# Optimization experiments

Hardware: AMD Instinct MI355X
Metric: run time of the kernel (lower is better)

Reference implementation:

```python
import jax, jax.numpy as jnp
import numpy as np

NUM_HEADS = 16

def setup_inputs() -> dict:
    key = jax.random.key(0)
    ks = jax.random.split(key, 11)
    S, B, E = 2048, 2, 1024
    scale = 1.0 / np.sqrt(E)
    return {
        "query": jax.random.normal(ks[0], (S, B, E), dtype=jnp.float32),
        "key":   jax.random.normal(ks[1], (S, B, E), dtype=jnp.float32),
        "value": jax.random.normal(ks[2], (S, B, E), dtype=jnp.float32),
        "Wq": jax.random.normal(ks[3], (E, E), dtype=jnp.float32) * scale,
        "bq": jax.random.normal(ks[4], (E,), dtype=jnp.float32) * 0.02,
        "Wk": jax.random.normal(ks[5], (E, E), dtype=jnp.float32) * scale,
        "bk": jax.random.normal(ks[6], (E,), dtype=jnp.float32) * 0.02,
        "Wv": jax.random.normal(ks[7], (E, E), dtype=jnp.float32) * scale,
        "bv": jax.random.normal(ks[8], (E,), dtype=jnp.float32) * 0.02,
        "Wo": jax.random.normal(ks[9], (E, E), dtype=jnp.float32) * scale,
        "bo": jax.random.normal(ks[10], (E,), dtype=jnp.float32) * 0.02,
    }

def _batch_invariant_softmax(x):
    # max-shift, exp in input dtype, sum/divide in float32, cast back
    x_max = jnp.max(x, axis=-1, keepdims=True)
    exp_x = jnp.exp(x - x_max).astype(jnp.float32)
    return (exp_x / jnp.sum(exp_x, axis=-1, keepdims=True)).astype(x.dtype)

def reference(query, key, value, Wq, bq, Wk, bk, Wv, bv, Wo, bo):
    S, B, E = query.shape
    H = NUM_HEADS
    D = E // H
    scale = 1.0 / np.sqrt(D)
    # projections (torch Linear: y = x @ W.T + b)
    q = query @ Wq.T + bq   # [S,B,E]
    k = key   @ Wk.T + bk
    v = value @ Wv.T + bv
    # [S,B,E] -> [B,H,S,D]
    q = q.reshape(S, B, H, D).transpose(1, 2, 0, 3)
    k = k.reshape(-1, B, H, D).transpose(1, 2, 0, 3)
    v = v.reshape(-1, B, H, D).transpose(1, 2, 0, 3)
    scores = jnp.einsum('bhqd,bhkd->bhqk', q, k) * scale  # [B,H,S,S]
    causal = jnp.triu(jnp.ones((S, S), dtype=bool), k=1)
    scores = jnp.where(causal, -jnp.inf, scores)
    attn = _batch_invariant_softmax(scores)
    out = jnp.einsum('bhqk,bhkd->bhqd', attn, v)  # [B,H,S,D]
    out = out.transpose(2, 0, 1, 3).reshape(S, B, E)  # [S,B,E]
    return out @ Wo.T + bo
```

## Files before the change

kernel.cpp:

```cpp
#include <hip/hip_runtime.h>
#include <cstddef>
#include <cstdint>

#define S_LEN 2048
#define B_SZ  2
#define E_SZ  1024
#define H_NUM 16
#define D_HEAD 64
#define M_ROWS 4096
#define NEG_BIG (-1e30f)

typedef __attribute__((ext_vector_type(8))) short bf16x8;
typedef __attribute__((ext_vector_type(4))) float f32x4;

#define P_QRYH (0ull << 20)
#define P_QRYL (8ull << 20)
#define P_KEYH (16ull << 20)
#define P_KEYL (24ull << 20)
#define P_VALH (32ull << 20)
#define P_VALL (40ull << 20)
#define P_WQH  (48ull << 20)
#define P_WQL  (50ull << 20)
#define P_WKH  (52ull << 20)
#define P_WKL  (54ull << 20)
#define P_WVH  (56ull << 20)
#define P_WVL  (58ull << 20)
#define P_WOH  (60ull << 20)
#define P_WOL  (62ull << 20)
#define P_QPH  (64ull << 20)
#define P_QPL  (72ull << 20)
#define P_KPH  (80ull << 20)
#define P_KPL  (88ull << 20)
#define P_VTH  (96ull << 20)
#define P_VTL  (104ull << 20)
#define P_AOH  (0ull << 20)
#define P_AOL  (8ull << 20)

__device__ __forceinline__ unsigned short rtne_bf16(float f) {
    unsigned int u = __float_as_uint(f);
    return (unsigned short)((u + 0x7fffu + ((u >> 16) & 1u)) >> 16);
}

__device__ __forceinline__ void split1(float f, unsigned short &h, unsigned short &l) {
    const unsigned int u = __float_as_uint(f);
    h = (unsigned short)(u >> 16);
    l = rtne_bf16(f - __uint_as_float(u & 0xffff0000u));
}

__device__ __forceinline__ void split4(const float4 v, ushort4 &h, ushort4 &l) {
    const unsigned int ux = __float_as_uint(v.x);
    const unsigned int uy = __float_as_uint(v.y);
    const unsigned int uz = __float_as_uint(v.z);
    const unsigned int uw = __float_as_uint(v.w);
    h.x = (unsigned short)(ux >> 16);
    h.y = (unsigned short)(uy >> 16);
    h.z = (unsigned short)(uz >> 16);
    h.w = (unsigned short)(uw >> 16);
    l.x = rtne_bf16(v.x - __uint_as_float(ux & 0xffff0000u));
    l.y = rtne_bf16(v.y - __uint_as_float(uy & 0xffff0000u));
    l.z = rtne_bf16(v.z - __uint_as_float(uz & 0xffff0000u));
    l.w = rtne_bf16(v.w - __uint_as_float(uw & 0xffff0000u));
}

__device__ __forceinline__ void gl16(const void* g, void* l) {
    __builtin_amdgcn_global_load_lds(
        (const __attribute__((address_space(1))) void*)g,
        (__attribute__((address_space(3))) void*)l, 16, 0, 0);
}

__global__ __launch_bounds__(256) void split_planes(
    const float* __restrict__ q, const float* __restrict__ k, const float* __restrict__ v,
    const float* __restrict__ wq, const float* __restrict__ wk,
    const float* __restrict__ wv, const float* __restrict__ wo,
    unsigned char* __restrict__ ws)
{
    const int z = blockIdx.y;
    const float* src; size_t oh, ol; int n;
    switch (z) {
        case 0: src = q;  oh = P_QRYH; ol = P_QRYL; n = 4194304; break;
        case 1: src = k;  oh = P_KEYH; ol = P_KEYL; n = 4194304; break;
        case 2: src = v;  oh = P_VALH; ol = P_VALL; n = 4194304; break;
        case 3: src = wq; oh = P_WQH;  ol = P_WQL;  n = 1048576; break;
        case 4: src = wk; oh = P_WKH;  ol = P_WKL;  n = 1048576; break;
        case 5: src = wv; oh = P_WVH;  ol = P_WVL;  n = 1048576; break;
        default:src = wo; oh = P_WOH;  ol = P_WOL;  n = 1048576; break;
    }
    const int i = blockIdx.x * 256 + threadIdx.x;
    if (i * 4 >= n) return;
    float4 vv = *(const float4*)&src[(size_t)i * 4];
    ushort4 h, l;
    split4(vv, h, l);
    *(ushort4*)(ws + oh + (size_t)i * 8) = h;
    *(ushort4*)(ws + ol + (size_t)i * 8) = l;
}

__global__ __launch_bounds__(256, 3) void gemm_qkv_planes(
    const float* __restrict__ bq, const float* __restrict__ bk, const float* __restrict__ bv,
    unsigned char* __restrict__ ws)
{
    __shared__ unsigned short AH[4096], AL[4096], WH[4096], WL[4096];

    const int z = blockIdx.z;
    const unsigned char* aph = ws + (z == 0 ? P_QRYH : z == 1 ? P_KEYH : P_VALH);
    const unsigned char* apl = ws + (z == 0 ? P_QRYL : z == 1 ? P_KEYL : P_VALL);
    const unsigned char* wph = ws + (z == 0 ? P_WQH : z == 1 ? P_WKH : P_WVH);
    const unsigned char* wpl = ws + (z == 0 ? P_WQL : z == 1 ? P_WKL : P_WVL);
    const float* bias = z == 0 ? bq : z == 1 ? bk : bv;
    const float postscale = (z == 0) ? 0.125f : 1.0f;

    const int t = threadIdx.x, lid = t & 63, w = t >> 6;
    const int wr = w >> 1, wc = w & 1, g = lid >> 4, r16 = lid & 15;
    const int m0 = blockIdx.x * 128, n0 = blockIdx.y * 128;

    const int lrow = lid >> 2;
    const int cA = (lid & 3) ^ (lrow & 3);

    int offA[4], offW[4];
#pragma unroll
    for (int m = 0; m < 4; ++m)
        offA[m] = (wr * 64 + m * 16 + r16) * 32 + ((g ^ (r16 & 3)) << 3);
#pragma unroll
    for (int n = 0; n < 4; ++n)
        offW[n] = (wc * 64 + n * 16 + r16) * 32 + ((g ^ (r16 & 3)) << 3);

    f32x4 acc[4][4];
    const f32x4 zero = {0.f, 0.f, 0.f, 0.f};
#pragma unroll
    for (int m = 0; m < 4; ++m)
#pragma unroll
        for (int n = 0; n < 4; ++n) acc[m][n] = zero;

    for (int kt = 0; kt < 1024; kt += 32) {
        __syncthreads();
#pragma unroll
        for (int i = 0; i < 2; ++i) {
            const int ra = m0 + w * 32 + i * 16 + lrow;
            const size_t ab = (size_t)ra * 2048 + (size_t)kt * 2 + (size_t)cA * 16;
            gl16(aph + ab, &AH[(w * 32 + i * 16) * 32]);
            gl16(apl + ab, &AL[(w * 32 + i * 16) * 32]);
            const int rw = n0 + w * 32 + i * 16 + lrow;
            const size_t wb = (size_t)rw * 2048 + (size_t)kt * 2 + (size_t)cA * 16;
            gl16(wph + wb, &WH[(w * 32 + i * 16) * 32]);
            gl16(wpl + wb, &WL[(w * 32 + i * 16) * 32]);
        }
        __syncthreads();

        bf16x8 ah[4], al[4], whf[4], wlf[4];
#pragma unroll
        for (int m = 0; m < 4; ++m) {
            ah[m] = *(const bf16x8*)&AH[offA[m]];
            al[m] = *(const bf16x8*)&AL[offA[m]];
        }
#pragma unroll
        for (int n = 0; n < 4; ++n) {
            whf[n] = *(const bf16x8*)&WH[offW[n]];
            wlf[n] = *(const bf16x8*)&WL[offW[n]];
        }
#pragma unroll
        for (int m = 0; m < 4; ++m)
#pragma unroll
            for (int n = 0; n < 4; ++n) {
                acc[m][n] = __builtin_amdgcn_mfma_f32_16x16x32_bf16(ah[m], whf[n], acc[m][n], 0, 0, 0);
                acc[m][n] = __builtin_amdgcn_mfma_f32_16x16x32_bf16(ah[m], wlf[n], acc[m][n], 0, 0, 0);
                acc[m][n] = __builtin_amdgcn_mfma_f32_16x16x32_bf16(al[m], whf[n], acc[m][n], 0, 0, 0);
            }
    }

    float bn[4];
#pragma unroll
    for (int n = 0; n < 4; ++n) bn[n] = bias[n0 + wc * 64 + n * 16 + r16];

    if (z < 2) {
        unsigned short* ph = (unsigned short*)(ws + (z == 0 ? P_QPH : P_KPH));
        unsigned short* pl = (unsigned short*)(ws + (z == 0 ? P_QPL : P_KPL));
#pragma unroll
        for (int m = 0; m < 4; ++m)
#pragma unroll
            for (int n = 0; n < 4; ++n) {
                const int col = n0 + wc * 64 + n * 16 + r16;
                const int hh = col >> 6, d = col & 63;
#pragma unroll
                for (int r = 0; r < 4; ++r) {
                    const int tok = m0 + wr * 64 + m * 16 + g * 4 + r;
                    const int s = tok >> 1, b = tok & 1;
                    unsigned short vh, vl;
                    split1((acc[m][n][r] + bn[n]) * postscale, vh, vl);
                    const size_t idx = ((size_t)((b * 16 + hh) * 2048 + s)) * 64 + d;
                    ph[idx] = vh; pl[idx] = vl;
                }
            }
    } else {
        unsigned short* ph = (unsigned short*)(ws + P_VTH);
        unsigned short* pl = (unsigned short*)(ws + P_VTL);
#pragma unroll
        for (int m = 0; m < 4; ++m)
#pragma unroll
            for (int n = 0; n < 4; ++n) {
                const int col = n0 + wc * 64 + n * 16 + r16;
                const int hh = col >> 6, d = col & 63;
                const int tok0 = m0 + wr * 64 + m * 16 + g * 4;
                const int s0 = tok0 >> 1;
                unsigned short vh[4], vl[4];
#pragma unroll
                for (int r = 0; r < 4; ++r) split1(acc[m][n][r] + bn[n], vh[r], vl[r]);
                const size_t i0 = ((size_t)((0  + hh) * 64 + d)) * 2048 + s0;
                const size_t i1 = ((size_t)((16 + hh) * 64 + d)) * 2048 + s0;
                ushort2 u;
                u.x = vh[0]; u.y = vh[2]; *(ushort2*)&ph[i0] = u;
                u.x = vh[1]; u.y = vh[3]; *(ushort2*)&ph[i1] = u;
                u.x = vl[0]; u.y = vl[2]; *(ushort2*)&pl[i0] = u;
                u.x = vl[1]; u.y = vl[3]; *(ushort2*)&pl[i1] = u;
            }
    }
}

__global__ __launch_bounds__(256, 2) void gemm_out_planes(
    const float* __restrict__ bo, const unsigned char* __restrict__ ws,
    float* __restrict__ out)
{
    __shared__ unsigned short AH[2048], AL[2048], WH[4096], WL[4096];

    const unsigned char* aph = ws + P_AOH;
    const unsigned char* apl = ws + P_AOL;
    const unsigned char* wph = ws + P_WOH;
    const unsigned char* wpl = ws + P_WOL;

    const int t = threadIdx.x, lid = t & 63, w = t >> 6;
    const int wr = w >> 1, wc = w & 1, g = lid >> 4, r16 = lid & 15;
    const int m0 = blockIdx.x * 64, n0 = blockIdx.y * 128;
    const int lrow = lid >> 2;
    const int cA = (lid & 3) ^ (lrow & 3);

    int offA[2], offW[4];
#pragma unroll
    for (int m = 0; m < 2; ++m)
        offA[m] = (wr * 32 + m * 16 + r16) * 32 + ((g ^ (r16 & 3)) << 3);
#pragma unroll
    for (int n = 0; n < 4; ++n)
        offW[n] = (wc * 64 + n * 16 + r16) * 32 + ((g ^ (r16 & 3)) << 3);

    f32x4 acc[2][4];
    const f32x4 zero = {0.f, 0.f, 0.f, 0.f};
#pragma unroll
    for (int m = 0; m < 2; ++m)
#pragma unroll
        for (int n = 0; n < 4; ++n) acc[m][n] = zero;

    for (int kt = 0; kt < 1024; kt += 32) {
        __syncthreads();
        {
            const int ra = m0 + w * 16 + lrow;
            const size_t ab = (size_t)ra * 2048 + (size_t)kt * 2 + (size_t)cA * 16;
            gl16(aph + ab, &AH[(w * 16) * 32]);
            gl16(apl + ab, &AL[(w * 16) * 32]);
        }
#pragma unroll
        for (int i = 0; i < 2; ++i) {
            const int rw = n0 + w * 32 + i * 16 + lrow;
            const size_t wb = (size_t)rw * 2048 + (size_t)kt * 2 + (size_t)cA * 16;
            gl16(wph + wb, &WH[(w * 32 + i * 16) * 32]);
            gl16(wpl + wb, &WL[(w * 32 + i * 16) * 32]);
        }
        __syncthreads();

        bf16x8 ah[2], al[2], whf[4], wlf[4];
#pragma unroll
        for (int m = 0; m < 2; ++m) {
            ah[m] = *(const bf16x8*)&AH[offA[m]];
            al[m] = *(const bf16x8*)&AL[offA[m]];
        }
#pragma unroll
        for (int n = 0; n < 4; ++n) {
            whf[n] = *(const bf16x8*)&WH[offW[n]];
            wlf[n] = *(const bf16x8*)&WL[offW[n]];
        }
#pragma unroll
        for (int m = 0; m < 2; ++m)
#pragma unroll
            for (int n = 0; n < 4; ++n) {
                acc[m][n] = __builtin_amdgcn_mfma_f32_16x16x32_bf16(ah[m], whf[n], acc[m][n], 0, 0, 0);
                acc[m][n] = __builtin_amdgcn_mfma_f32_16x16x32_bf16(ah[m], wlf[n], acc[m][n], 0, 0, 0);
                acc[m][n] = __builtin_amdgcn_mfma_f32_16x16x32_bf16(al[m], whf[n], acc[m][n], 0, 0, 0);
            }
    }

    float bn[4];
#pragma unroll
    for (int n = 0; n < 4; ++n) bn[n] = bo[n0 + wc * 64 + n * 16 + r16];
#pragma unroll
    for (int m = 0; m < 2; ++m)
#pragma unroll
        for (int n = 0; n < 4; ++n) {
            const int col = n0 + wc * 64 + n * 16 + r16;
#pragma unroll
            for (int r = 0; r < 4; ++r) {
                const int row = m0 + wr * 32 + m * 16 + g * 4 + r;
                out[(size_t)row * 1024 + col] = acc[m][n][r] + bn[n];
            }
        }
}

__global__ __launch_bounds__(256, 2) void attn_fwd(unsigned char* __restrict__ ws)
{
    __shared__ unsigned short sm[40960];

    const int t = threadIdx.x, lid = t & 63, w = t >> 6;
    const int g = lid >> 4, r16 = lid & 15;

    const int c = blockIdx.x;
    const int logical = (c & 7) * 64 + (c >> 3);
    const int bh = logical >> 4;
    const int xq = logical & 15;
    const int b = bh >> 4, h = bh & 15;

    const unsigned char* qhp  = ws + P_QPH + (size_t)bh * 262144;
    const unsigned char* qlp  = ws + P_QPL + (size_t)bh * 262144;
    const unsigned char* khp  = ws + P_KPH + (size_t)bh * 262144;
    const unsigned char* klp  = ws + P_KPL + (size_t)bh * 262144;
    const unsigned char* vthp = ws + P_VTH + (size_t)bh * 262144;
    const unsigned char* vtlp = ws + P_VTL + (size_t)bh * 262144;
    unsigned short* aoh = (unsigned short*)(ws + P_AOH);
    unsigned short* aol = (unsigned short*)(ws + P_AOL);

    const int lrow = lid >> 3;
    const int cK = (lid & 7) ^ lrow;

    int offF[4][2], offQ[2], offP[4][4];
#pragma unroll
    for (int nf = 0; nf < 4; ++nf)
#pragma unroll
        for (int ks = 0; ks < 2; ++ks)
            offF[nf][ks] = (nf * 16 + r16) * 64 + (((ks * 4 + g) ^ (r16 & 7)) << 3);
#pragma unroll
    for (int ks = 0; ks < 2; ++ks)
        offQ[ks] = (w * 16 + r16) * 64 + (((ks * 4 + g) ^ (r16 & 7)) << 3);
#pragma unroll
    for (int nf = 0; nf < 4; ++nf)
#pragma unroll
        for (int r = 0; r < 4; ++r) {
            const int rp = w * 16 + g * 4 + r;
            offP[nf][r] = rp * 64 + (((nf * 2 + (r16 >> 3)) ^ (rp & 7)) << 3) + (r16 & 7);
        }

    auto stage_kv = [&](int bsel, int tt) {
#pragma unroll
        for (int i = 0; i < 2; ++i) {
            const int r = w * 16 + i * 8 + lrow;
            const int db = bsel * 16384 + (w * 16 + i * 8) * 64;
            const size_t kb = (size_t)(tt * 64 + r) * 128 + (size_t)cK * 16;
            gl16(khp + kb, &sm[db]);
            gl16(klp + kb, &sm[db + 4096]);
            const size_t vb = (size_t)r * 4096 + (size_t)tt * 128 + (size_t)cK * 16;
            gl16(vthp + vb, &sm[db + 8192]);
            gl16(vtlp + vb, &sm[db + 12288]);
        }
    };

    const f32x4 zero = {0.f, 0.f, 0.f, 0.f};

    for (int pass = 0; pass < 2; ++pass) {
        const int qt = (pass == 0) ? xq : 31 - xq;
        const int q0 = qt * 64;

#pragma unroll
        for (int i = 0; i < 2; ++i) {
            const int r = w * 16 + i * 8 + lrow;
            const size_t qb = (size_t)(q0 + r) * 128 + (size_t)cK * 16;
            gl16(qhp + qb, &sm[32768 + (w * 16 + i * 8) * 64]);
            gl16(qlp + qb, &sm[36864 + (w * 16 + i * 8) * 64]);
        }
        stage_kv(0, 0);
        __syncthreads();

        bf16x8 qh[2], ql[2];
#pragma unroll
        for (int ks = 0; ks < 2; ++ks) {
            qh[ks] = *(const bf16x8*)&sm[32768 + offQ[ks]];
            ql[ks] = *(const bf16x8*)&sm[36864 + offQ[ks]];
        }

        f32x4 oacc[4];
        float l_r[4];
#pragma unroll
        for (int i = 0; i < 4; ++i) { oacc[i] = zero; l_r[i] = 0.f; }

        for (int tt = 0; tt <= qt; ++tt) {
            const int bb = (tt & 1) * 16384;
            if (tt < qt) stage_kv((tt & 1) ^ 1, tt + 1);

            f32x4 sacc[4];
#pragma unroll
            for (int nf = 0; nf < 4; ++nf) sacc[nf] = zero;
            __builtin_amdgcn_s_setprio(1);
#pragma unroll
            for (int nf = 0; nf < 4; ++nf)
#pragma unroll
                for (int ks = 0; ks < 2; ++ks) {
                    bf16x8 kh = *(const bf16x8*)&sm[bb + offF[nf][ks]];
                    bf16x8 kl = *(const bf16x8*)&sm[bb + 4096 + offF[nf][ks]];
                    sacc[nf] = __builtin_amdgcn_mfma_f32_16x16x32_bf16(qh[ks], kh, sacc[nf], 0, 0, 0);
                    sacc[nf] = __builtin_amdgcn_mfma_f32_16x16x32_bf16(qh[ks], kl, sacc[nf], 0, 0, 0);
                    sacc[nf] = __builtin_amdgcn_mfma_f32_16x16x32_bf16(ql[ks], kh, sacc[nf], 0, 0, 0);
                }
            __builtin_amdgcn_s_setprio(0);

            if (tt == qt) {
#pragma unroll
                for (int nf = 0; nf < 4; ++nf) {
                    const int k_loc = nf * 16 + r16;
#pragma unroll
                    for (int r = 0; r < 4; ++r) {
                        const int q_loc = w * 16 + g * 4 + r;
                        if (k_loc > q_loc) sacc[nf][r] = NEG_BIG;
                    }
                }
            }

            float pv4[4][4];
#pragma unroll
            for (int nf = 0; nf < 4; ++nf)
#pragma unroll
                for (int r = 0; r < 4; ++r) {
                    const float p = __expf(sacc[nf][r]);
                    pv4[nf][r] = p;
                    l_r[r] += p;
                }

#pragma unroll
            for (int nf = 0; nf < 4; ++nf)
#pragma unroll
                for (int r = 0; r < 4; ++r) {
                    unsigned short h1, l1;
                    split1(pv4[nf][r], h1, l1);
                    sm[32768 + offP[nf][r]] = h1;
                    sm[36864 + offP[nf][r]] = l1;
                }

            __builtin_amdgcn_s_setprio(1);
#pragma unroll
            for (int ks = 0; ks < 2; ++ks) {
                bf16x8 pah = *(const bf16x8*)&sm[32768 + offQ[ks]];
                bf16x8 pal = *(const bf16x8*)&sm[36864 + offQ[ks]];
#pragma unroll
                for (int nf = 0; nf < 4; ++nf) {
                    bf16x8 vh = *(const bf16x8*)&sm[bb + 8192 + offF[nf][ks]];
                    bf16x8 vl = *(const bf16x8*)&sm[bb + 12288 + offF[nf][ks]];
                    oacc[nf] = __builtin_amdgcn_mfma_f32_16x16x32_bf16(pah, vh, oacc[nf], 0, 0, 0);
                    oacc[nf] = __builtin_amdgcn_mfma_f32_16x16x32_bf16(pah, vl, oacc[nf], 0, 0, 0);
                    oacc[nf] = __builtin_amdgcn_mfma_f32_16x16x32_bf16(pal, vh, oacc[nf], 0, 0, 0);
                }
            }
            __builtin_amdgcn_s_setprio(0);
            __syncthreads();
        }

#pragma unroll
        for (int off = 1; off < 16; off <<= 1)
#pragma unroll
            for (int r = 0; r < 4; ++r)
                l_r[r] += __shfl_xor(l_r[r], off, 64);

        float inv[4];
#pragma unroll
        for (int r = 0; r < 4; ++r) inv[r] = 1.0f / l_r[r];
#pragma unroll
        for (int nf = 0; nf < 4; ++nf) {
            const int d = nf * 16 + r16;
#pragma unroll
            for (int r = 0; r < 4; ++r) {
                const int s = q0 + w * 16 + g * 4 + r;
                unsigned short hh, ll;
                split1(oacc[nf][r] * inv[r], hh, ll);
                const size_t idx = (size_t)(s * 2 + b) * 1024 + h * 64 + d;
                aoh[idx] = hh; aol[idx] = ll;
            }
        }
    }
}

extern "C" void kernel_launch(void* const* d_in, const int* in_sizes, int n_in,
                              void* d_out, int out_size, void* d_ws, size_t ws_size,
                              hipStream_t stream)
{
    const float* query = (const float*)d_in[0];
    const float* key   = (const float*)d_in[1];
    const float* value = (const float*)d_in[2];
    const float* Wq = (const float*)d_in[3];  const float* bq = (const float*)d_in[4];
    const float* Wk = (const float*)d_in[5];  const float* bk = (const float*)d_in[6];
    const float* Wv = (const float*)d_in[7];  const float* bv = (const float*)d_in[8];
    const float* Wo = (const float*)d_in[9];  const float* bo = (const float*)d_in[10];
    float* out = (float*)d_out;
    unsigned char* ws = (unsigned char*)d_ws;
    (void)ws_size; (void)in_sizes; (void)n_in; (void)out_size;

    const dim3 tb(256);

    split_planes<<<dim3(4096, 7), tb, 0, stream>>>(query, key, value, Wq, Wk, Wv, Wo, ws);
    gemm_qkv_planes<<<dim3(32, 8, 3), tb, 0, stream>>>(bq, bk, bv, ws);
    attn_fwd<<<dim3(512), tb, 0, stream>>>(ws);
    gemm_out_planes<<<dim3(64, 8), tb, 0, stream>>>(bo, ws, out);
}
```

Measured before the change: 317.4 us.

## Double-buffer LDS tiles in projection GEMMs with async prefetch and MFMA priority

Both split-bf16 GEMM kernels now keep two LDS buffers and issue the global-to-LDS loads for the next K tile before computing on the current one. This lets memory latency overlap MFMA work and drops one barrier per iteration. It also raises wave priority around the MFMA block. The cost is doubled shared memory, so the QKV kernel's launch-bounds occupancy target drops from 3 to 2, while the output GEMM's target is raised to 3.

```diff
diff --git a/kernel.cpp b/kernel.cpp
--- a/kernel.cpp
+++ b/kernel.cpp
@@ -94,11 +94,11 @@
     *(ushort4*)(ws + ol + (size_t)i * 8) = l;
 }
 
-__global__ __launch_bounds__(256, 3) void gemm_qkv_planes(
+__global__ __launch_bounds__(256, 2) void gemm_qkv_planes(
     const float* __restrict__ bq, const float* __restrict__ bk, const float* __restrict__ bv,
     unsigned char* __restrict__ ws)
 {
-    __shared__ unsigned short AH[4096], AL[4096], WH[4096], WL[4096];
+    __shared__ unsigned short SM[2 * 16384];
 
     const int z = blockIdx.z;
     const unsigned char* aph = ws + (z == 0 ? P_QRYH : z == 1 ? P_KEYH : P_VALH);
@@ -123,6 +123,21 @@
     for (int n = 0; n < 4; ++n)
         offW[n] = (wc * 64 + n * 16 + r16) * 32 + ((g ^ (r16 & 3)) << 3);
 
+    auto stage = [&](int bsel, int kt) {
+        const int B = bsel * 16384;
+#pragma unroll
+        for (int i = 0; i < 2; ++i) {
+            const int ra = m0 + w * 32 + i * 16 + lrow;
+            const size_t ab = (size_t)ra * 2048 + (size_t)kt * 64 + (size_t)cA * 16;
+            gl16(aph + ab, &SM[B + (w * 32 + i * 16) * 32]);
+            gl16(apl + ab, &SM[B + 4096 + (w * 32 + i * 16) * 32]);
+            const int rw = n0 + w * 32 + i * 16 + lrow;
+            const size_t wb = (size_t)rw * 2048 + (size_t)kt * 64 + (size_t)cA * 16;
+            gl16(wph + wb, &SM[B + 8192 + (w * 32 + i * 16) * 32]);
+            gl16(wpl + wb, &SM[B + 12288 + (w * 32 + i * 16) * 32]);
+        }
+    };
+
     f32x4 acc[4][4];
     const f32x4 zero = {0.f, 0.f, 0.f, 0.f};
 #pragma unroll
@@ -130,32 +145,25 @@
 #pragma unroll
         for (int n = 0; n < 4; ++n) acc[m][n] = zero;
 
-    for (int kt = 0; kt < 1024; kt += 32) {
-        __syncthreads();
-#pragma unroll
-        for (int i = 0; i < 2; ++i) {
-            const int ra = m0 + w * 32 + i * 16 + lrow;
-            const size_t ab = (size_t)ra * 2048 + (size_t)kt * 2 + (size_t)cA * 16;
-            gl16(aph + ab, &AH[(w * 32 + i * 16) * 32]);
-            gl16(apl + ab, &AL[(w * 32 + i * 16) * 32]);
-            const int rw = n0 + w * 32 + i * 16 + lrow;
-            const size_t wb = (size_t)rw * 2048 + (size_t)kt * 2 + (size_t)cA * 16;
-            gl16(wph + wb, &WH[(w * 32 + i * 16) * 32]);
-            gl16(wpl + wb, &WL[(w * 32 + i * 16) * 32]);
-        }
-        __syncthreads();
+    stage(0, 0);
+    __syncthreads();
+
+    for (int kt = 0; kt < 32; ++kt) {
+        const int cur = (kt & 1) * 16384;
+        if (kt + 1 < 32) stage((kt & 1) ^ 1, kt + 1);
 
         bf16x8 ah[4], al[4], whf[4], wlf[4];
 #pragma unroll
         for (int m = 0; m < 4; ++m) {
-            ah[m] = *(const bf16x8*)&AH[offA[m]];
-            al[m] = *(const bf16x8*)&AL[offA[m]];
+            ah[m] = *(const bf16x8*)&SM[cur + offA[m]];
+            al[m] = *(const bf16x8*)&SM[cur + 4096 + offA[m]];
         }
 #pragma unroll
         for (int n = 0; n < 4; ++n) {
-            whf[n] = *(const bf16x8*)&WH[offW[n]];
-            wlf[n] = *(const bf16x8*)&WL[offW[n]];
-        }
+            whf[n] = *(const bf16x8*)&SM[cur + 8192 + offW[n]];
+            wlf[n] = *(const bf16x8*)&SM[cur + 12288 + offW[n]];
+        }
+        __builtin_amdgcn_s_setprio(1);
 #pragma unroll
         for (int m = 0; m < 4; ++m)
 #pragma unroll
@@ -164,6 +172,8 @@
                 acc[m][n] = __builtin_amdgcn_mfma_f32_16x16x32_bf16(ah[m], wlf[n], acc[m][n], 0, 0, 0);
                 acc[m][n] = __builtin_amdgcn_mfma_f32_16x16x32_bf16(al[m], whf[n], acc[m][n], 0, 0, 0);
             }
+        __builtin_amdgcn_s_setprio(0);
+        __syncthreads();
     }
 
     float bn[4];
@@ -214,11 +224,11 @@
     }
 }
 
-__global__ __launch_bounds__(256, 2) void gemm_out_planes(
+__global__ __launch_bounds__(256, 3) void gemm_out_planes(
     const float* __restrict__ bo, const unsigned char* __restrict__ ws,
     float* __restrict__ out)
 {
-    __shared__ unsigned short AH[2048], AL[2048], WH[4096], WL[4096];
+    __shared__ unsigned short SM[2 * 12288];
 
     const unsigned char* aph = ws + P_AOH;
     const unsigned char* apl = ws + P_AOL;
@@ -239,6 +249,23 @@
     for (int n = 0; n < 4; ++n)
         offW[n] = (wc * 64 + n * 16 + r16) * 32 + ((g ^ (r16 & 3)) << 3);
 
+    auto stage = [&](int bsel, int kt) {
+        const int B = bsel * 12288;
+        {
+            const int ra = m0 + w * 16 + lrow;
+            const size_t ab = (size_t)ra * 2048 + (size_t)kt * 64 + (size_t)cA * 16;
+            gl16(aph + ab, &SM[B + (w * 16) * 32]);
+            gl16(apl + ab, &SM[B + 2048 + (w * 16) * 32]);
+        }
+#pragma unroll
+        for (int i = 0; i < 2; ++i) {
+            const int rw = n0 + w * 32 + i * 16 + lrow;
+            const size_t wb = (size_t)rw * 2048 + (size_t)kt * 64 + (size_t)cA * 16;
+            gl16(wph + wb, &SM[B + 4096 + (w * 32 + i * 16) * 32]);
+            gl16(wpl + wb, &SM[B + 8192 + (w * 32 + i * 16) * 32]);
+        }
+    };
+
     f32x4 acc[2][4];
     const f32x4 zero = {0.f, 0.f, 0.f, 0.f};
 #pragma unroll
@@ -246,34 +273,25 @@
 #pragma unroll
         for (int n = 0; n < 4; ++n) acc[m][n] = zero;
 
-    for (int kt = 0; kt < 1024; kt += 32) {
-        __syncthreads();
-        {
-            const int ra = m0 + w * 16 + lrow;
-            const size_t ab = (size_t)ra * 2048 + (size_t)kt * 2 + (size_t)cA * 16;
-            gl16(aph + ab, &AH[(w * 16) * 32]);
-            gl16(apl + ab, &AL[(w * 16) * 32]);
-        }
-#pragma unroll
-        for (int i = 0; i < 2; ++i) {
-            const int rw = n0 + w * 32 + i * 16 + lrow;
-            const size_t wb = (size_t)rw * 2048 + (size_t)kt * 2 + (size_t)cA * 16;
-            gl16(wph + wb, &WH[(w * 32 + i * 16) * 32]);
-            gl16(wpl + wb, &WL[(w * 32 + i * 16) * 32]);
-        }
-        __syncthreads();
+    stage(0, 0);
+    __syncthreads();
+
+    for (int kt = 0; kt < 32; ++kt) {
+        const int cur = (kt & 1) * 12288;
+        if (kt + 1 < 32) stage((kt & 1) ^ 1, kt + 1);
 
         bf16x8 ah[2], al[2], whf[4], wlf[4];
 #pragma unroll
         for (int m = 0; m < 2; ++m) {
-            ah[m] = *(const bf16x8*)&AH[offA[m]];
-            al[m] = *(const bf16x8*)&AL[offA[m]];
+            ah[m] = *(const bf16x8*)&SM[cur + offA[m]];
+            al[m] = *(const bf16x8*)&SM[cur + 2048 + offA[m]];
         }
 #pragma unroll
         for (int n = 0; n < 4; ++n) {
-            whf[n] = *(const bf16x8*)&WH[offW[n]];
-            wlf[n] = *(const bf16x8*)&WL[offW[n]];
-        }
+            whf[n] = *(const bf16x8*)&SM[cur + 4096 + offW[n]];
+            wlf[n] = *(const bf16x8*)&SM[cur + 8192 + offW[n]];
+        }
+        __builtin_amdgcn_s_setprio(1);
 #pragma unroll
         for (int m = 0; m < 2; ++m)
 #pragma unroll
@@ -282,6 +300,8 @@
                 acc[m][n] = __builtin_amdgcn_mfma_f32_16x16x32_bf16(ah[m], wlf[n], acc[m][n], 0, 0, 0);
                 acc[m][n] = __builtin_amdgcn_mfma_f32_16x16x32_bf16(al[m], whf[n], acc[m][n], 0, 0, 0);
             }
+        __builtin_amdgcn_s_setprio(0);
+        __syncthreads();
     }
 
     float bn[4];
```

Measured after the change: 302.2 us. 1.05x faster.
